# Optimization experiments

Hardware: AMD Instinct MI355X
Metric: run time of the kernel (lower is better)

## Reference

```python
import jax, jax.numpy as jnp
import numpy as np

HIDDEN = 1024
HEADS = 16
HEAD_DIM = HIDDEN // HEADS


def setup_inputs() -> dict:
    key = jax.random.key(0)
    k1, k2, k3, k4, k5 = jax.random.split(key, 5)
    scale = 1.0 / np.sqrt(HIDDEN)
    return {
        "query": jax.random.normal(k1, (8, 1024, HIDDEN), dtype=jnp.float32),
        "w_qkv": jax.random.normal(k2, (HIDDEN, 3 * HIDDEN), dtype=jnp.float32) * scale,
        "b_qkv": jnp.zeros((3 * HIDDEN,), dtype=jnp.float32),
        "w_o": jax.random.normal(k3, (HIDDEN, HIDDEN), dtype=jnp.float32) * scale,
        "b_o": jnp.zeros((HIDDEN,), dtype=jnp.float32),
    }


def reference(query, w_qkv, b_qkv, w_o, b_o):
    B, S, _ = query.shape
    qkv = query @ w_qkv + b_qkv                      # [B,S,3H]
    q, k, v = jnp.split(qkv, 3, axis=-1)
    # split heads -> [B, heads, S, head_dim]
    def sh(x):
        return x.reshape(B, S, HEADS, HEAD_DIM).transpose(0, 2, 1, 3)
    qh, kh, vh = sh(q), sh(k), sh(v)
    qh = qh * (HEAD_DIM ** -0.5)
    logits = jnp.einsum("bhqd,bhkd->bhqk", qh, kh)   # [B,H,S,S]
    weights = jax.nn.softmax(logits, axis=-1)        # dropout p=0.0 -> identity
    x = jnp.einsum("bhqk,bhkd->bhqd", weights, vh)
    x = x.transpose(0, 2, 1, 3).reshape(B, S, HIDDEN)
    return x @ w_o + b_o
```

## Files before the change

### kernel.cpp

```cpp
#include <hip/hip_runtime.h>
#include <math.h>

#define BATCH   8
#define SEQ     1024
#define HIDDEN  1024
#define NHEADS  16
#define HDIM    64
#define MROWS   (BATCH * SEQ)

typedef __bf16 bf16x8 __attribute__((ext_vector_type(8)));
typedef float  f32x4  __attribute__((ext_vector_type(4)));

__device__ __forceinline__ unsigned short f2bf(float f) {
    union { float f; unsigned int u; } v; v.f = f;
    unsigned int u = v.u;
    u += 0x7fffu + ((u >> 16) & 1u);
    return (unsigned short)(u >> 16);
}

__device__ __forceinline__ unsigned int pack2bf_trunc(float a, float b) {
    union { float f; unsigned int u; } ua, ub;
    ua.f = a; ub.f = b;
    return (ua.u >> 16) | (ub.u & 0xFFFF0000u);
}

__device__ __forceinline__ void gl2lds16(const unsigned short* g, unsigned short* l) {
    __builtin_amdgcn_global_load_lds(
        (const __attribute__((address_space(1))) void*)g,
        (__attribute__((address_space(3))) void*)l, 16, 0, 0);
}

__global__ __launch_bounds__(256) void prep_kernel(
    const float* __restrict__ query, unsigned short* __restrict__ queryBf,
    const float* __restrict__ wqkv,  unsigned short* __restrict__ wqkvT,
    const float* __restrict__ wo,    unsigned short* __restrict__ woT) {
    __shared__ float tile[32][33];
    const int bid = blockIdx.x;
    const int tid = threadIdx.x;

    if (bid < 8192) {
        int i = bid * 256 + tid;
        float4 v = reinterpret_cast<const float4*>(query)[i];
        ushort4 o;
        o.x = f2bf(v.x); o.y = f2bf(v.y); o.z = f2bf(v.z); o.w = f2bf(v.w);
        reinterpret_cast<ushort4*>(queryBf)[i] = o;
        return;
    }

    const float* in;
    unsigned short* out;
    int R, C, bx, by;
    if (bid < 8192 + 3072) {
        int b = bid - 8192;
        in = wqkv; out = wqkvT; R = HIDDEN; C = 3 * HIDDEN;
        bx = b % 96; by = b / 96;
    } else {
        int b = bid - 11264;
        in = wo; out = woT; R = HIDDEN; C = HIDDEN;
        bx = b % 32; by = b / 32;
    }
    const int tx = tid & 31, ty = tid >> 5;
    const int x  = bx * 32 + tx;
    const int y0 = by * 32;
#pragma unroll
    for (int j = 0; j < 32; j += 8)
        tile[ty + j][tx] = in[(size_t)(y0 + ty + j) * C + x];
    __syncthreads();
    const int x2 = y0 + tx;
    const int y2 = bx * 32;
#pragma unroll
    for (int j = 0; j < 32; j += 8)
        out[(size_t)(y2 + ty + j) * R + x2] = f2bf(tile[tx][ty + j]);
}

template <int EPI>
__global__ __launch_bounds__(256) void gemm_bt_kernel(
    const unsigned short* __restrict__ A,
    const unsigned short* __restrict__ Bt,
    const float* __restrict__ bias,
    unsigned short* __restrict__ out_bf,
    float* __restrict__ out_f,
    int M, int N, int K) {
    __shared__ __align__(16) unsigned short As[128 * 64];
    __shared__ __align__(16) unsigned short Bs[128 * 64];

    const int tid  = threadIdx.x;
    const int wid  = tid >> 6;
    const int lane = tid & 63;
    const int l15  = lane & 15;
    const int quad = lane >> 4;
    const int wm   = (wid & 1) * 64;
    const int wn   = (wid >> 1) * 64;

    const int npn = N >> 7;
    const int pid = blockIdx.x;
    const int ppg = 4 * npn;
    const int gid = pid / ppg;
    const int loc = pid - gid * ppg;
    const int pm  = gid * 4 + (loc & 3);
    const int pn  = loc >> 2;
    const int m0  = pm * 128;
    const int n0  = pn * 128;

    const int srow = wid * 32 + (lane >> 3);
    const int skcs = ((lane & 7) ^ (lane >> 3)) * 8;
    const int rsw  = lane & 7;

    f32x4 acc[4][4];
#pragma unroll
    for (int i = 0; i < 4; ++i)
#pragma unroll
        for (int j = 0; j < 4; ++j) acc[i][j] = (f32x4){0.f, 0.f, 0.f, 0.f};

    for (int kt = 0; kt < K; kt += 64) {
        __syncthreads();
#pragma unroll
        for (int it = 0; it < 4; ++it) {
            int row = srow + it * 8;
            gl2lds16(A  + (size_t)(m0 + row) * K + kt + skcs, As + (wid * 32 + it * 8) * 64);
            gl2lds16(Bt + (size_t)(n0 + row) * K + kt + skcs, Bs + (wid * 32 + it * 8) * 64);
        }
        __syncthreads();
#pragma unroll
        for (int ks = 0; ks < 2; ++ks) {
            bf16x8 afr[4], bfr[4];
#pragma unroll
            for (int i = 0; i < 4; ++i)
                afr[i] = *reinterpret_cast<const bf16x8*>(
                    As + (wm + i * 16 + l15) * 64 + ((ks * 4 + quad) ^ rsw) * 8);
#pragma unroll
            for (int j = 0; j < 4; ++j)
                bfr[j] = *reinterpret_cast<const bf16x8*>(
                    Bs + (wn + j * 16 + l15) * 64 + ((ks * 4 + quad) ^ rsw) * 8);
#pragma unroll
            for (int i = 0; i < 4; ++i)
#pragma unroll
                for (int j = 0; j < 4; ++j)
                    acc[i][j] = __builtin_amdgcn_mfma_f32_16x16x32_bf16(afr[i], bfr[j], acc[i][j], 0, 0, 0);
        }
    }

#pragma unroll
    for (int j = 0; j < 4; ++j) {
        int col   = n0 + wn + j * 16 + l15;
        float bv  = bias[col];
        if constexpr (EPI == 0) {
            int which = col >> 10;
            int rem   = col & 1023;
            int h     = rem >> 6, d = rem & 63;
            if (which == 2) {
#pragma unroll
                for (int i = 0; i < 4; ++i) {
                    int row0 = m0 + wm + i * 16 + quad * 4;
                    int b    = row0 >> 10, s0 = row0 & 1023;
                    ushort4 o;
                    o.x = f2bf(acc[i][j][0] + bv);
                    o.y = f2bf(acc[i][j][1] + bv);
                    o.z = f2bf(acc[i][j][2] + bv);
                    o.w = f2bf(acc[i][j][3] + bv);
                    size_t idx = ((size_t)(2 * BATCH * NHEADS) +
                                  (size_t)b * NHEADS + h) * (SEQ * HDIM) +
                                 (size_t)d * SEQ + s0;
                    *reinterpret_cast<ushort4*>(out_bf + idx) = o;
                }
            } else {
                float sc = (which == 0) ? 0.18033688011112042f : 1.0f;
#pragma unroll
                for (int i = 0; i < 4; ++i)
#pragma unroll
                    for (int r = 0; r < 4; ++r) {
                        int row = m0 + wm + i * 16 + quad * 4 + r;
                        int b   = row >> 10, s = row & 1023;
                        float v = (acc[i][j][r] + bv) * sc;
                        size_t idx = ((((size_t)which * BATCH + b) * NHEADS + h) * SEQ + s) * HDIM + d;
                        out_bf[idx] = f2bf(v);
                    }
            }
        } else {
#pragma unroll
            for (int i = 0; i < 4; ++i)
#pragma unroll
                for (int r = 0; r < 4; ++r) {
                    int row = m0 + wm + i * 16 + quad * 4 + r;
                    out_f[(size_t)row * N + col] = acc[i][j][r] + bv;
                }
        }
    }
}

__global__ __launch_bounds__(256, 4) void attn_kernel(
    const unsigned short* __restrict__ qkv,
    const unsigned short* __restrict__ vt,
    unsigned short* __restrict__ x) {
    constexpr int LDP = 68;
    __shared__ __align__(16) unsigned short Ks[64 * 64];
    __shared__ __align__(16) unsigned short Vs[64 * 64];
    __shared__ __align__(16) unsigned short PQ[4][32 * LDP];

    unsigned short* Qs = &PQ[0][0];

    const int tid  = threadIdx.x;
    const int wid  = tid >> 6;
    const int lane = tid & 63;
    const int l15  = lane & 15;
    const int quad = lane >> 4;
    const int srow8 = lane >> 3;
    const int skcs  = ((lane & 7) ^ srow8) * 8;
    const int rsw   = lane & 7;

    const int id = blockIdx.x;
    const int bh = (id & 7) * 16 + (id >> 6);
    const int q0 = ((id >> 3) & 7) * 128;

    const unsigned short* Qg  = qkv + (size_t)bh * SEQ * HDIM;
    const unsigned short* Kg  = qkv + (size_t)(128 + bh) * SEQ * HDIM;
    const unsigned short* VTg = vt + (size_t)bh * SEQ * HDIM;

#pragma unroll
    for (int it = 0; it < 4; ++it) {
        gl2lds16(Qg + (size_t)(q0 + wid * 32 + it * 8 + srow8) * HDIM + skcs,
                 Qs + (wid * 32 + it * 8) * 64);
    }
    __syncthreads();

    bf16x8 qf[2][2];
#pragma unroll
    for (int m = 0; m < 2; ++m)
#pragma unroll
        for (int h = 0; h < 2; ++h)
            qf[m][h] = *reinterpret_cast<const bf16x8*>(
                Qs + (wid * 32 + m * 16 + l15) * 64 + ((h * 4 + quad) ^ rsw) * 8);

    float lsum[2][4];
    f32x4 accO[2][4];
#pragma unroll
    for (int m = 0; m < 2; ++m)
#pragma unroll
        for (int r = 0; r < 4; ++r) lsum[m][r] = 0.f;
#pragma unroll
    for (int m = 0; m < 2; ++m)
#pragma unroll
        for (int jd = 0; jd < 4; ++jd) accO[m][jd] = (f32x4){0.f, 0.f, 0.f, 0.f};

    for (int t0 = 0; t0 < SEQ; t0 += 64) {
        __syncthreads();
#pragma unroll
        for (int it = 0; it < 2; ++it) {
            int row = wid * 16 + it * 8 + srow8;
            int sK = ((lane & 7) ^ (wid * 2 + it)) * 8;
            gl2lds16(Kg + (size_t)(t0 + row) * HDIM + sK, Ks + (wid * 16 + it * 8) * 64);
            gl2lds16(VTg + (size_t)row * SEQ + t0 + skcs,   Vs + (wid * 16 + it * 8) * 64);
        }
        __syncthreads();

        f32x4 accL[2][4];
#pragma unroll
        for (int m = 0; m < 2; ++m)
#pragma unroll
            for (int j = 0; j < 4; ++j) accL[m][j] = (f32x4){0.f, 0.f, 0.f, 0.f};
#pragma unroll
        for (int j = 0; j < 4; ++j) {
            int krow = l15 * 4 + j;
            int kru  = krow >> 3;
            bf16x8 kf0 = *reinterpret_cast<const bf16x8*>(
                Ks + krow * 64 + ((0 + quad) ^ kru) * 8);
            bf16x8 kf1 = *reinterpret_cast<const bf16x8*>(
                Ks + krow * 64 + ((4 + quad) ^ kru) * 8);
#pragma unroll
            for (int m = 0; m < 2; ++m) {
                accL[m][j] = __builtin_amdgcn_mfma_f32_16x16x32_bf16(qf[m][0], kf0, accL[m][j], 0, 0, 0);
                accL[m][j] = __builtin_amdgcn_mfma_f32_16x16x32_bf16(qf[m][1], kf1, accL[m][j], 0, 0, 0);
            }
        }

#pragma unroll
        for (int m = 0; m < 2; ++m)
#pragma unroll
            for (int r = 0; r < 4; ++r) {
                float p0 = exp2f(accL[m][0][r]);
                float p1 = exp2f(accL[m][1][r]);
                float p2 = exp2f(accL[m][2][r]);
                float p3 = exp2f(accL[m][3][r]);
                lsum[m][r] += (p0 + p1) + (p2 + p3);
                uint2 pk;
                pk.x = pack2bf_trunc(p0, p1);
                pk.y = pack2bf_trunc(p2, p3);
                *reinterpret_cast<uint2*>(
                    &PQ[wid][(m * 16 + quad * 4 + r) * LDP + l15 * 4]) = pk;
            }

        bf16x8 pf[2][2];
#pragma unroll
        for (int m = 0; m < 2; ++m)
#pragma unroll
            for (int h = 0; h < 2; ++h)
                pf[m][h] = *reinterpret_cast<const bf16x8*>(
                    PQ[wid] + (m * 16 + l15) * LDP + h * 32 + quad * 8);
#pragma unroll
        for (int jd = 0; jd < 4; ++jd) {
            bf16x8 vf0 = *reinterpret_cast<const bf16x8*>(
                Vs + (jd * 16 + l15) * 64 + ((0 + quad) ^ rsw) * 8);
            bf16x8 vf1 = *reinterpret_cast<const bf16x8*>(
                Vs + (jd * 16 + l15) * 64 + ((4 + quad) ^ rsw) * 8);
#pragma unroll
            for (int m = 0; m < 2; ++m) {
                accO[m][jd] = __builtin_amdgcn_mfma_f32_16x16x32_bf16(pf[m][0], vf0, accO[m][jd], 0, 0, 0);
                accO[m][jd] = __builtin_amdgcn_mfma_f32_16x16x32_bf16(pf[m][1], vf1, accO[m][jd], 0, 0, 0);
            }
        }
    }

    const int b = bh >> 4, h = bh & 15;
#pragma unroll
    for (int m = 0; m < 2; ++m)
#pragma unroll
        for (int r = 0; r < 4; ++r) {
            float s = lsum[m][r];
            s += __shfl_xor(s, 1);
            s += __shfl_xor(s, 2);
            s += __shfl_xor(s, 4);
            s += __shfl_xor(s, 8);
            float inv = 1.0f / s;
            int srow = q0 + wid * 32 + m * 16 + quad * 4 + r;
            size_t base = ((size_t)b * SEQ + srow) * HIDDEN + h * HDIM;
#pragma unroll
            for (int jd = 0; jd < 4; ++jd)
                x[base + jd * 16 + l15] = f2bf(accO[m][jd][r] * inv);
        }
}

extern "C" void kernel_launch(void* const* d_in, const int* in_sizes, int n_in,
                              void* d_out, int out_size, void* d_ws, size_t ws_size,
                              hipStream_t stream) {
    const float* query = (const float*)d_in[0];
    const float* w_qkv = (const float*)d_in[1];
    const float* b_qkv = (const float*)d_in[2];
    const float* w_o   = (const float*)d_in[3];
    const float* b_o   = (const float*)d_in[4];
    float* out = (float*)d_out;

    unsigned short* ws = (unsigned short*)d_ws;
    unsigned short* queryBf = ws;
    unsigned short* wqkvT   = queryBf + (size_t)MROWS * HIDDEN;
    unsigned short* woT     = wqkvT + (size_t)3 * HIDDEN * HIDDEN;
    unsigned short* qkvbuf  = woT + (size_t)HIDDEN * HIDDEN;
    unsigned short* xbuf    = qkvbuf + (size_t)3 * MROWS * HIDDEN;
    unsigned short* vtbuf   = qkvbuf + (size_t)2 * BATCH * NHEADS * SEQ * HDIM;

    prep_kernel<<<dim3(12288), 256, 0, stream>>>(
        query, queryBf, w_qkv, wqkvT, w_o, woT);

    gemm_bt_kernel<0><<<dim3((MROWS / 128) * (3 * HIDDEN / 128)), 256, 0, stream>>>(
        queryBf, wqkvT, b_qkv, qkvbuf, nullptr, MROWS, 3 * HIDDEN, HIDDEN);

    attn_kernel<<<dim3(1024), 256, 0, stream>>>(qkvbuf, vtbuf, xbuf);

    gemm_bt_kernel<1><<<dim3((MROWS / 128) * (HIDDEN / 128)), 256, 0, stream>>>(
        xbuf, woT, b_o, nullptr, out, MROWS, HIDDEN, HIDDEN);
}
```

Before: 238.4 us.

## Double-buffer K/V tiles in attention and use hardware exp2 intrinsic

Doubles the K and V shared-memory tiles so the next tile's global-to-LDS load is issued before computing on the current tile. This replaces two barriers per iteration with one, aiming to hide load latency. It also switches exp2f to the raw hardware exp2 builtin to skip range handling. Shared memory use grows and the launch bound drops to 3 blocks per CU, which lowers occupancy.

```diff
diff --git a/kernel.cpp b/kernel.cpp
--- a/kernel.cpp
+++ b/kernel.cpp
@@ -188,13 +188,13 @@
     }
 }
 
-__global__ __launch_bounds__(256, 4) void attn_kernel(
+__global__ __launch_bounds__(256, 3) void attn_kernel(
     const unsigned short* __restrict__ qkv,
     const unsigned short* __restrict__ vt,
     unsigned short* __restrict__ x) {
     constexpr int LDP = 68;
-    __shared__ __align__(16) unsigned short Ks[64 * 64];
-    __shared__ __align__(16) unsigned short Vs[64 * 64];
+    __shared__ __align__(16) unsigned short Ks[2][64 * 64];
+    __shared__ __align__(16) unsigned short Vs[2][64 * 64];
     __shared__ __align__(16) unsigned short PQ[4][32 * LDP];
 
     unsigned short* Qs = &PQ[0][0];
@@ -216,11 +216,24 @@
     const unsigned short* Kg  = qkv + (size_t)(128 + bh) * SEQ * HDIM;
     const unsigned short* VTg = vt + (size_t)bh * SEQ * HDIM;
 
+    auto stageKV = [&](int t0s, int buf) {
+#pragma unroll
+        for (int it = 0; it < 2; ++it) {
+            int row = wid * 16 + it * 8 + srow8;
+            int sK = ((lane & 7) ^ (wid * 2 + it)) * 8;
+            gl2lds16(Kg + (size_t)(t0s + row) * HDIM + sK,
+                     Ks[buf] + (wid * 16 + it * 8) * 64);
+            gl2lds16(VTg + (size_t)row * SEQ + t0s + skcs,
+                     Vs[buf] + (wid * 16 + it * 8) * 64);
+        }
+    };
+
 #pragma unroll
     for (int it = 0; it < 4; ++it) {
         gl2lds16(Qg + (size_t)(q0 + wid * 32 + it * 8 + srow8) * HDIM + skcs,
                  Qs + (wid * 32 + it * 8) * 64);
     }
+    stageKV(0, 0);
     __syncthreads();
 
     bf16x8 qf[2][2];
@@ -230,6 +243,7 @@
         for (int h = 0; h < 2; ++h)
             qf[m][h] = *reinterpret_cast<const bf16x8*>(
                 Qs + (wid * 32 + m * 16 + l15) * 64 + ((h * 4 + quad) ^ rsw) * 8);
+    __syncthreads();
 
     float lsum[2][4];
     f32x4 accO[2][4];
@@ -243,15 +257,8 @@
         for (int jd = 0; jd < 4; ++jd) accO[m][jd] = (f32x4){0.f, 0.f, 0.f, 0.f};
 
     for (int t0 = 0; t0 < SEQ; t0 += 64) {
-        __syncthreads();
-#pragma unroll
-        for (int it = 0; it < 2; ++it) {
-            int row = wid * 16 + it * 8 + srow8;
-            int sK = ((lane & 7) ^ (wid * 2 + it)) * 8;
-            gl2lds16(Kg + (size_t)(t0 + row) * HDIM + sK, Ks + (wid * 16 + it * 8) * 64);
-            gl2lds16(VTg + (size_t)row * SEQ + t0 + skcs,   Vs + (wid * 16 + it * 8) * 64);
-        }
-        __syncthreads();
+        const int cur = (t0 >> 6) & 1;
+        if (t0 + 64 < SEQ) stageKV(t0 + 64, cur ^ 1);
 
         f32x4 accL[2][4];
 #pragma unroll
@@ -263,9 +270,9 @@
             int krow = l15 * 4 + j;
             int kru  = krow >> 3;
             bf16x8 kf0 = *reinterpret_cast<const bf16x8*>(
-                Ks + krow * 64 + ((0 + quad) ^ kru) * 8);
+                Ks[cur] + krow * 64 + ((0 + quad) ^ kru) * 8);
             bf16x8 kf1 = *reinterpret_cast<const bf16x8*>(
-                Ks + krow * 64 + ((4 + quad) ^ kru) * 8);
+                Ks[cur] + krow * 64 + ((4 + quad) ^ kru) * 8);
 #pragma unroll
             for (int m = 0; m < 2; ++m) {
                 accL[m][j] = __builtin_amdgcn_mfma_f32_16x16x32_bf16(qf[m][0], kf0, accL[m][j], 0, 0, 0);
@@ -277,10 +284,10 @@
         for (int m = 0; m < 2; ++m)
 #pragma unroll
             for (int r = 0; r < 4; ++r) {
-                float p0 = exp2f(accL[m][0][r]);
-                float p1 = exp2f(accL[m][1][r]);
-                float p2 = exp2f(accL[m][2][r]);
-                float p3 = exp2f(accL[m][3][r]);
+                float p0 = __builtin_amdgcn_exp2f(accL[m][0][r]);
+                float p1 = __builtin_amdgcn_exp2f(accL[m][1][r]);
+                float p2 = __builtin_amdgcn_exp2f(accL[m][2][r]);
+                float p3 = __builtin_amdgcn_exp2f(accL[m][3][r]);
                 lsum[m][r] += (p0 + p1) + (p2 + p3);
                 uint2 pk;
                 pk.x = pack2bf_trunc(p0, p1);
@@ -299,15 +306,17 @@
 #pragma unroll
         for (int jd = 0; jd < 4; ++jd) {
             bf16x8 vf0 = *reinterpret_cast<const bf16x8*>(
-                Vs + (jd * 16 + l15) * 64 + ((0 + quad) ^ rsw) * 8);
+                Vs[cur] + (jd * 16 + l15) * 64 + ((0 + quad) ^ rsw) * 8);
             bf16x8 vf1 = *reinterpret_cast<const bf16x8*>(
-                Vs + (jd * 16 + l15) * 64 + ((4 + quad) ^ rsw) * 8);
+                Vs[cur] + (jd * 16 + l15) * 64 + ((4 + quad) ^ rsw) * 8);
 #pragma unroll
             for (int m = 0; m < 2; ++m) {
                 accO[m][jd] = __builtin_amdgcn_mfma_f32_16x16x32_bf16(pf[m][0], vf0, accO[m][jd], 0, 0, 0);
                 accO[m][jd] = __builtin_amdgcn_mfma_f32_16x16x32_bf16(pf[m][1], vf1, accO[m][jd], 0, 0, 0);
             }
         }
+
+        __syncthreads();
     }
 
     const int b = bh >> 4, h = bh & 15;
```

Result: no change. 237.4 us (-0.4%).

## Prefetch next K/V tile into registers during attention compute

Applied to the files above, without the earlier changes.

Each iteration of the attention loop now loads the next K and V^T tile from global memory into registers before computing the current tile. After the compute it writes them to LDS between two barriers, replacing the direct global-to-LDS loads that stalled each step. The first tile is loaded in the prologue alongside Q. The exp2f calls are also swapped for the hardware exp2 builtin. Register pressure goes up, and the hand-computed LDS destination offsets have to reproduce the layout the old gl2lds16 path produced.

```diff
diff --git a/kernel.cpp b/kernel.cpp
--- a/kernel.cpp
+++ b/kernel.cpp
@@ -216,11 +216,24 @@
     const unsigned short* Kg  = qkv + (size_t)(128 + bh) * SEQ * HDIM;
     const unsigned short* VTg = vt + (size_t)bh * SEQ * HDIM;
 
+    const int r0   = wid * 16 + srow8;
+    const int r1   = r0 + 8;
+    const int sK0  = ((lane & 7) ^ (wid * 2 + 0)) * 8;
+    const int sK1  = ((lane & 7) ^ (wid * 2 + 1)) * 8;
+    unsigned short* ldsK0 = Ks + (wid * 16 + 0) * 64 + lane * 8;
+    unsigned short* ldsK1 = Ks + (wid * 16 + 8) * 64 + lane * 8;
+    unsigned short* ldsV0 = Vs + (wid * 16 + 0) * 64 + lane * 8;
+    unsigned short* ldsV1 = Vs + (wid * 16 + 8) * 64 + lane * 8;
+
 #pragma unroll
     for (int it = 0; it < 4; ++it) {
         gl2lds16(Qg + (size_t)(q0 + wid * 32 + it * 8 + srow8) * HDIM + skcs,
                  Qs + (wid * 32 + it * 8) * 64);
     }
+    gl2lds16(Kg + (size_t)r0 * HDIM + sK0, Ks + (wid * 16 + 0) * 64);
+    gl2lds16(Kg + (size_t)r1 * HDIM + sK1, Ks + (wid * 16 + 8) * 64);
+    gl2lds16(VTg + (size_t)r0 * SEQ + skcs, Vs + (wid * 16 + 0) * 64);
+    gl2lds16(VTg + (size_t)r1 * SEQ + skcs, Vs + (wid * 16 + 8) * 64);
     __syncthreads();
 
     bf16x8 qf[2][2];
@@ -230,6 +243,7 @@
         for (int h = 0; h < 2; ++h)
             qf[m][h] = *reinterpret_cast<const bf16x8*>(
                 Qs + (wid * 32 + m * 16 + l15) * 64 + ((h * 4 + quad) ^ rsw) * 8);
+    __syncthreads();
 
     float lsum[2][4];
     f32x4 accO[2][4];
@@ -242,16 +256,17 @@
 #pragma unroll
         for (int jd = 0; jd < 4; ++jd) accO[m][jd] = (f32x4){0.f, 0.f, 0.f, 0.f};
 
+    uint4 kr0, kr1, vr0, vr1;
+
     for (int t0 = 0; t0 < SEQ; t0 += 64) {
-        __syncthreads();
-#pragma unroll
-        for (int it = 0; it < 2; ++it) {
-            int row = wid * 16 + it * 8 + srow8;
-            int sK = ((lane & 7) ^ (wid * 2 + it)) * 8;
-            gl2lds16(Kg + (size_t)(t0 + row) * HDIM + sK, Ks + (wid * 16 + it * 8) * 64);
-            gl2lds16(VTg + (size_t)row * SEQ + t0 + skcs,   Vs + (wid * 16 + it * 8) * 64);
-        }
-        __syncthreads();
+        const bool pf_next = (t0 + 64 < SEQ);
+        if (pf_next) {
+            const int tn = t0 + 64;
+            kr0 = *reinterpret_cast<const uint4*>(Kg + (size_t)(tn + r0) * HDIM + sK0);
+            kr1 = *reinterpret_cast<const uint4*>(Kg + (size_t)(tn + r1) * HDIM + sK1);
+            vr0 = *reinterpret_cast<const uint4*>(VTg + (size_t)r0 * SEQ + tn + skcs);
+            vr1 = *reinterpret_cast<const uint4*>(VTg + (size_t)r1 * SEQ + tn + skcs);
+        }
 
         f32x4 accL[2][4];
 #pragma unroll
@@ -277,10 +292,10 @@
         for (int m = 0; m < 2; ++m)
 #pragma unroll
             for (int r = 0; r < 4; ++r) {
-                float p0 = exp2f(accL[m][0][r]);
-                float p1 = exp2f(accL[m][1][r]);
-                float p2 = exp2f(accL[m][2][r]);
-                float p3 = exp2f(accL[m][3][r]);
+                float p0 = __builtin_amdgcn_exp2f(accL[m][0][r]);
+                float p1 = __builtin_amdgcn_exp2f(accL[m][1][r]);
+                float p2 = __builtin_amdgcn_exp2f(accL[m][2][r]);
+                float p3 = __builtin_amdgcn_exp2f(accL[m][3][r]);
                 lsum[m][r] += (p0 + p1) + (p2 + p3);
                 uint2 pk;
                 pk.x = pack2bf_trunc(p0, p1);
@@ -308,6 +323,15 @@
                 accO[m][jd] = __builtin_amdgcn_mfma_f32_16x16x32_bf16(pf[m][1], vf1, accO[m][jd], 0, 0, 0);
             }
         }
+
+        __syncthreads();
+        if (pf_next) {
+            *reinterpret_cast<uint4*>(ldsK0) = kr0;
+            *reinterpret_cast<uint4*>(ldsK1) = kr1;
+            *reinterpret_cast<uint4*>(ldsV0) = vr0;
+            *reinterpret_cast<uint4*>(ldsV1) = vr1;
+        }
+        __syncthreads();
     }
 
     const int b = bh >> 4, h = bh & 15;
```

Measured after the change: 291.8 us. 22.4% more time.
